# Performance work log

Hardware: AMD Instinct MI355X
Metric: run time of the kernel (lower is better)

Reference implementation:

```python
import jax, jax.numpy as jnp
import numpy as np

# dims
B, F, K = 64, 4096, 8
D_IN = D_SLOT = D_KVQ = 192
HID = 768
N_ITERS = 3
EPS = 1e-8
GROUPS = [(0, 1), (1, 7), (7, 8)]  # bg / fg / ag contiguous slot slices
SB_STRENGTH = 1.0
SB_SIGMA = 0.25
GRID = 64  # sqrt(F)


def _layernorm(x, g, b):
    m = jnp.mean(x, axis=-1, keepdims=True)
    v = jnp.mean(jnp.square(x - m), axis=-1, keepdims=True)
    return (x - m) * jax.lax.rsqrt(v + 1e-5) * g + b


def _gru_cell(x, h, Wih, Whh, bih, bhh):
    # torch.nn.GRUCell semantics; gate order r, z, n
    gi = x @ Wih.T + bih
    gh = h @ Whh.T + bhh
    ir, iz, i_n = jnp.split(gi, 3, axis=-1)
    hr, hz, h_n = jnp.split(gh, 3, axis=-1)
    r = jax.nn.sigmoid(ir + hr)
    z = jax.nn.sigmoid(iz + hz)
    n = jnp.tanh(i_n + r * h_n)
    return (1.0 - z) * n + z * h


def _token_coords():
    y = np.linspace(-1.0, 1.0, GRID, dtype=np.float32)
    x = np.linspace(-1.0, 1.0, GRID, dtype=np.float32)
    yy, xx = np.meshgrid(y, x, indexing='ij')
    return jnp.asarray(np.stack((xx, yy), axis=-1).reshape(F, 2))


def setup_inputs() -> dict:
    key = jax.random.key(0)
    ks = jax.random.split(key, 16)
    def n(i, shape, s=0.02):
        return jax.random.normal(ks[i], shape, jnp.float32) * s
    return dict(
        features=jax.random.normal(ks[0], (B, F, D_IN), jnp.float32),
        slots=jax.random.normal(ks[1], (B, K, D_SLOT), jnp.float32),
        Wk=n(2, (D_IN, D_KVQ)), Wv=n(3, (D_IN, D_KVQ)), Wq=n(4, (D_SLOT, D_KVQ)),
        ln_feat_g=jnp.ones(D_IN), ln_feat_b=jnp.zeros(D_IN),
        ln_slot_g=jnp.ones(D_SLOT), ln_slot_b=jnp.zeros(D_SLOT),
        gru_Wih=n(5, (3, 3 * D_SLOT, D_KVQ)), gru_Whh=n(6, (3, 3 * D_SLOT, D_SLOT)),
        gru_bih=n(7, (3, 3 * D_SLOT)), gru_bhh=n(8, (3, 3 * D_SLOT)),
        mlp_ln_g=jnp.ones((3, D_SLOT)), mlp_ln_b=jnp.zeros((3, D_SLOT)),
        mlp_W1=n(9, (3, D_SLOT, HID)), mlp_b1=n(10, (3, HID)),
        mlp_W2=n(11, (3, HID, D_SLOT)), mlp_b2=n(12, (3, D_SLOT)),
    )


def reference(features, slots, Wk, Wv, Wq, ln_feat_g, ln_feat_b, ln_slot_g,
              ln_slot_b, gru_Wih, gru_Whh, gru_bih, gru_bhh, mlp_ln_g,
              mlp_ln_b, mlp_W1, mlp_b1, mlp_W2, mlp_b2):
    coords = _token_coords()  # (F, 2)
    f = _layernorm(features, ln_feat_g, ln_feat_b)
    k = f @ Wk  # (B, F, Dk)
    v = f @ Wv
    scale = D_KVQ ** -0.5
    sigma2 = max(SB_SIGMA ** 2, 1e-8)
    prev_attn = None
    for _ in range(N_ITERS):
        slots_prev = slots
        q = _layernorm(slots, ln_slot_g, ln_slot_b) @ Wq  # (B, K, Dk)
        dots = jnp.einsum('bkd,bfd->bkf', q, k) * scale
        if prev_attn is not None and SB_STRENGTH > 0.0:
            w = prev_attn / (prev_attn.sum(-1, keepdims=True) + 1e-8)
            centers = jnp.einsum('bkf,fd->bkd', w, coords)  # (B, K, 2)
            diff = coords[None, None] - centers[:, :, None]  # (B, K, F, 2)
            dist2 = jnp.sum(diff * diff, axis=-1)
            dots = dots + SB_STRENGTH * (-dist2 / (2.0 * sigma2))
        attn = jax.nn.softmax(dots, axis=1)  # competition over slots
        prev_attn = attn
        w = attn / (attn.sum(-1, keepdims=True) + EPS)  # weighted mean over F
        updates = jnp.einsum('bkf,bfd->bkd', w, v)  # (B, K, Dk)
        outs = []
        for g, (s, e) in enumerate(GROUPS):
            u = updates[:, s:e].reshape(-1, D_KVQ)
            h_prev = slots_prev[:, s:e].reshape(-1, D_SLOT)
            h = _gru_cell(u, h_prev, gru_Wih[g], gru_Whh[g], gru_bih[g], gru_bhh[g])
            x = _layernorm(h, mlp_ln_g[g], mlp_ln_b[g])
            x = jax.nn.relu(x @ mlp_W1[g] + mlp_b1[g]) @ mlp_W2[g] + mlp_b2[g]
            outs.append((h + x).reshape(B, e - s, D_SLOT))
        slots = jnp.concatenate(outs, axis=1)
    return slots
```

## Files before the change

### kernel.cpp

```cpp
#include <hip/hip_runtime.h>

typedef unsigned short u16;
typedef unsigned int u32;

#define BB 64
#define FF 4096
#define DD 192
#define HH 768

typedef __attribute__((ext_vector_type(8))) __bf16 bf16x8;
typedef __attribute__((ext_vector_type(4))) float f32x4;

__device__ __forceinline__ float bf2f(u32 u) {
  union { u32 i; float f; } x; x.i = u << 16; return x.f;
}
__device__ __forceinline__ u16 f2bf(float f) {
  __bf16 h = (__bf16)f;
  return __builtin_bit_cast(u16, h);
}
__device__ __forceinline__ u32 pk2bf(float a, float b) {
  return (u32)f2bf(a) | ((u32)f2bf(b) << 16);
}
__device__ __forceinline__ float sigm(float x) { return 1.f / (1.f + __expf(-x)); }

__global__ void prep_wmod(const float* __restrict__ Wk, const float* __restrict__ Wv,
                          const float* __restrict__ g, const float* __restrict__ bb,
                          u16* __restrict__ wmodT, float* __restrict__ s1,
                          float* __restrict__ s0) {
  int n = blockIdx.x * 64 + threadIdx.x;
  const float* W = (n < DD) ? Wk : Wv;
  int col = (n < DD) ? n : n - DD;
  float a1 = 0.f, a0 = 0.f;
  for (int e = 0; e < DD; ++e) {
    float w = W[e * DD + col];
    u16 h = f2bf(g[e] * w);
    wmodT[n * DD + e] = h;
    a1 += bf2f(h);
    a0 += bb[e] * w;
  }
  s1[n] = a1; s0[n] = a0;
}

__global__ void prep_packw(const float* __restrict__ Wih, const float* __restrict__ Whh,
                           const float* __restrict__ W1, const float* __restrict__ W2,
                           u16* __restrict__ pWih, u16* __restrict__ pWhh,
                           u16* __restrict__ pW1, u16* __restrict__ pW2) {
  int which = blockIdx.y;
  int total, N, E;
  const float* src; u16* dst; int srcEmajor;
  if (which < 2) { total = 3 * 576 * 192; N = 576; E = 192; srcEmajor = 0;
                   src = which ? Whh : Wih; dst = which ? pWhh : pWih; }
  else if (which == 2) { total = 3 * 192 * 768; N = 768; E = 192; srcEmajor = 1;
                         src = W1; dst = pW1; }
  else { total = 3 * 768 * 192; N = 192; E = 768; srcEmajor = 1; src = W2; dst = pW2; }
  for (int idx = blockIdx.x * 256 + threadIdx.x; idx < total; idx += gridDim.x * 256) {
    int g = idx / (N * E), rem = idx % (N * E);
    int n, e;
    if (srcEmajor) { e = rem / N; n = rem % N; }
    else { n = rem / E; e = rem % E; }
    dst[((g * (E / 2) + (e >> 1)) * N + n) * 2 + (e & 1)] = f2bf(src[idx]);
  }
}

__global__ __launch_bounds__(256, 4) void proj_kernel(
    const float* __restrict__ feat, const u16* __restrict__ wmodT,
    const float* __restrict__ s1v, const float* __restrict__ s0v,
    u16* __restrict__ kc_, u16* __restrict__ vc_) {
  __shared__ __align__(16) u16 Ctile[4][2176];
  int tid = threadIdx.x;
  int w = tid >> 6, lane = tid & 63;
  int l15 = lane & 15, l4 = lane >> 4;
  long wtile = (long)blockIdx.x * 4 + w;
  long tok0 = wtile * 16;
  int bidx = (int)(wtile >> 8);
  int f0 = ((int)wtile & 255) * 16;
  char* ct = (char*)&Ctile[w][0];

  const float* fp = feat + (tok0 + l15) * DD + l4 * 8;
  float4 xa[6], xb[6];
  #pragma unroll
  for (int kk = 0; kk < 6; ++kk) {
    xa[kk] = *(const float4*)(fp + kk * 32);
    xb[kk] = *(const float4*)(fp + kk * 32 + 4);
  }
  float s = 0.f, s2 = 0.f;
  bf16x8 afr[6];
  #pragma unroll
  for (int kk = 0; kk < 6; ++kk) {
    float4 a = xa[kk], b = xb[kk];
    s += a.x + a.y + a.z + a.w + b.x + b.y + b.z + b.w;
    s2 += a.x * a.x + a.y * a.y + a.z * a.z + a.w * a.w +
          b.x * b.x + b.y * b.y + b.z * b.z + b.w * b.w;
    union { u32 u[4]; bf16x8 v; } cv;
    cv.u[0] = pk2bf(a.x, a.y); cv.u[1] = pk2bf(a.z, a.w);
    cv.u[2] = pk2bf(b.x, b.y); cv.u[3] = pk2bf(b.z, b.w);
    afr[kk] = cv.v;
  }
  s += __shfl_xor(s, 16); s2 += __shfl_xor(s2, 16);
  s += __shfl_xor(s, 32); s2 += __shfl_xor(s2, 32);
  float mu = s * (1.f / 192.f);
  float rstd = rsqrtf(s2 * (1.f / 192.f) - mu * mu + 1e-5f);
  float muv[4], rsv[4];
  #pragma unroll
  for (int j = 0; j < 4; ++j) {
    muv[j] = __shfl(mu, l4 * 4 + j);
    rsv[j] = __shfl(rstd, l4 * 4 + j);
  }

  #pragma unroll 1
  for (int grp = 0; grp < 4; ++grp) {
    f32x4 acc[6];
    #pragma unroll
    for (int nt = 0; nt < 6; ++nt) acc[nt] = (f32x4){0.f, 0.f, 0.f, 0.f};
    #pragma unroll
    for (int kk = 0; kk < 6; ++kk) {
      #pragma unroll
      for (int nt = 0; nt < 6; ++nt) {
        int col = grp * 96 + nt * 16 + l15;
        bf16x8 bfr = *(const bf16x8*)(wmodT + col * DD + kk * 32 + l4 * 8);
        acc[nt] = __builtin_amdgcn_mfma_f32_16x16x32_bf16(afr[kk], bfr, acc[nt], 0, 0, 0);
      }
    }
    if (grp < 2) {
      #pragma unroll
      for (int nt = 0; nt < 6; ++nt) {
        int col = nt * 16 + l15;
        float s1c = s1v[grp * 96 + col], s0c = s0v[grp * 96 + col];
        #pragma unroll
        for (int j = 0; j < 4; ++j) {
          int tau = l4 * 4 + j;
          u16 hv = f2bf(rsv[j] * (acc[nt][j] - muv[j] * s1c) + s0c);
          *(u16*)(ct + tau * 272 + (col >> 3) * 16 + (col & 7) * 2) = hv;
        }
      }
      #pragma unroll
      for (int it = 0; it < 3; ++it) {
        int fi = lane + it * 64;
        int g = fi >> 4, tau = fi & 15;
        uint4 val = *(uint4*)(ct + tau * 272 + g * 16);
        *(uint4*)(kc_ + (((long)wtile * 24 + grp * 12 + g) * 16 + tau) * 8) = val;
      }
    } else {
      #pragma unroll
      for (int nt = 0; nt < 6; ++nt) {
        int col = (grp - 2) * 96 + nt * 16 + l15;
        float s1c = s1v[col + 192], s0c = s0v[col + 192];
        int ntg = col >> 4;
        uint2 pk;
        pk.x = pk2bf(rsv[0] * (acc[nt][0] - muv[0] * s1c) + s0c,
                     rsv[1] * (acc[nt][1] - muv[1] * s1c) + s0c);
        pk.y = pk2bf(rsv[2] * (acc[nt][2] - muv[2] * s1c) + s0c,
                     rsv[3] * (acc[nt][3] - muv[3] * s1c) + s0c);
        u32 ox = __shfl_xor((int)pk.x, 16);
        u32 oy = __shfl_xor((int)pk.y, 16);
        if ((l4 & 1) == 0) {
          int t0 = f0 + l4 * 4;
          int g32 = t0 >> 5;
          int l4f = (t0 >> 3) & 3;
          uint4 val = {pk.x, pk.y, ox, oy};
          *(uint4*)(vc_ + ((((long)bidx * 128 + g32) * 12 + ntg) * 64 + l4f * 16 +
                           (col & 15)) * 8) = val;
        }
      }
    }
  }
}

__global__ __launch_bounds__(64) void qproj_kernel(
    const float* __restrict__ slots, const float* __restrict__ Wq,
    const float* __restrict__ g, const float* __restrict__ bb,
    float* __restrict__ qbuf, float* __restrict__ upd,
    float* __restrict__ asum_cur, float* __restrict__ cacc_cur) {
  __shared__ float ln[192];
  int bk = blockIdx.x;
  int lane = threadIdx.x;
  {
    int gtid = bk * 64 + lane;
    float4 z = {0.f, 0.f, 0.f, 0.f};
    if (gtid < 24576) ((float4*)upd)[gtid] = z;
    else if (gtid < 24576 + 128) ((float4*)asum_cur)[gtid - 24576] = z;
    else if (gtid < 24576 + 384) ((float4*)cacc_cur)[gtid - 24704] = z;
  }
  const float* x = slots + bk * DD;
  float v0 = x[lane], v1 = x[lane + 64], v2 = x[lane + 128];
  float s = v0 + v1 + v2, s2 = v0 * v0 + v1 * v1 + v2 * v2;
  #pragma unroll
  for (int m = 1; m < 64; m <<= 1) { s += __shfl_xor(s, m); s2 += __shfl_xor(s2, m); }
  float mu = s * (1.f / 192.f);
  float rstd = rsqrtf(s2 * (1.f / 192.f) - mu * mu + 1e-5f);
  ln[lane]       = (v0 - mu) * rstd * g[lane]       + bb[lane];
  ln[lane + 64]  = (v1 - mu) * rstd * g[lane + 64]  + bb[lane + 64];
  ln[lane + 128] = (v2 - mu) * rstd * g[lane + 128] + bb[lane + 128];
  __syncthreads();
  float a0 = 0.f, a1 = 0.f, a2 = 0.f;
  for (int e = 0; e < DD; ++e) {
    float le = ln[e];
    a0 += le * Wq[e * DD + lane];
    a1 += le * Wq[e * DD + lane + 64];
    a2 += le * Wq[e * DD + lane + 128];
  }
  const float scale = 0.07216878364870323f;
  qbuf[bk * DD + lane]       = a0 * scale;
  qbuf[bk * DD + lane + 64]  = a1 * scale;
  qbuf[bk * DD + lane + 128] = a2 * scale;
}

__global__ __launch_bounds__(256) void attnupd_kernel(
    const u16* __restrict__ kc_, const u16* __restrict__ vc_,
    const float* __restrict__ qbuf,
    const float* __restrict__ asum_prev, const float* __restrict__ cacc_prev,
    float* __restrict__ upd, float* __restrict__ asum_cur,
    float* __restrict__ cacc_cur, int have_bias) {
  __shared__ __align__(16) u16 qlds[16 * 192];
  __shared__ __align__(16) u16 attn_lds[16 * 256];
  int b = blockIdx.x;
  int chunk = blockIdx.y * 256;
  int tid = threadIdx.x;
  if (tid < 192) {
    int s = tid / 24, u = tid % 24;
    const float* qp = qbuf + (b * 8 + s) * DD + u * 8;
    uint4 p;
    p.x = pk2bf(qp[0], qp[1]);
    p.y = pk2bf(qp[2], qp[3]);
    p.z = pk2bf(qp[4], qp[5]);
    p.w = pk2bf(qp[6], qp[7]);
    *(uint4*)((char*)qlds + s * 384 + ((u ^ (s & 7)) << 4)) = p;
  } else {
    int t2 = tid - 192;
    #pragma unroll
    for (int i = 0; i < 3; ++i) {
      int idx = t2 * 3 + i;
      int s = 8 + idx / 24, u = idx % 24;
      *(uint4*)((char*)qlds + s * 384 + ((u ^ (s & 7)) << 4)) = (uint4){0, 0, 0, 0};
    }
    #pragma unroll
    for (int i = 0; i < 4; ++i)
      *(uint4*)((char*)attn_lds + 4096 + (t2 * 4 + i) * 16) = (uint4){0, 0, 0, 0};
  }
  __syncthreads();
  int w = tid >> 6, lane = tid & 63;
  int l15 = lane & 15, l4 = lane >> 4;
  bf16x8 qfr[6];
  #pragma unroll
  for (int kk = 0; kk < 6; ++kk) {
    int u = kk * 4 + l4;
    qfr[kk] = *(bf16x8*)((char*)qlds + l15 * 384 + ((u ^ (l15 & 7)) << 4));
  }
  float ax[4], ay[4], c0[4];
  #pragma unroll
  for (int j = 0; j < 4; ++j) {
    int s = l4 * 4 + j;
    if (have_bias && s < 8) {
      float inv = 1.f / (asum_prev[b * 8 + s] + 1e-8f);
      float cx = cacc_prev[(b * 8 + s) * 2] * inv;
      float cy = cacc_prev[(b * 8 + s) * 2 + 1] * inv;
      ax[j] = 16.f * cx; ay[j] = 16.f * cy; c0[j] = -8.f * (cx * cx + cy * cy);
    } else { ax[j] = 0.f; ay[j] = 0.f; c0[j] = 0.f; }
  }
  float pa[4], px[4], py[4];
  #pragma unroll
  for (int j = 0; j < 4; ++j) { pa[j] = 0.f; px[j] = 0.f; py[j] = 0.f; }
  for (int tile = w; tile < 16; tile += 4) {
    int t0 = chunk + tile * 16;
    long Tg = (long)b * 256 + (t0 >> 4);
    const u16* kp = kc_ + (Tg * 24 + l4) * 128 + l15 * 8;
    f32x4 acc = (f32x4){0.f, 0.f, 0.f, 0.f};
    #pragma unroll
    for (int kk = 0; kk < 6; ++kk) {
      bf16x8 bfr = *(const bf16x8*)(kp + kk * 512);
      acc = __builtin_amdgcn_mfma_f32_16x16x32_bf16(qfr[kk], bfr, acc, 0, 0, 0);
    }
    int t = t0 + l15;
    float x = -1.f + (float)(t & 63) * (2.f / 63.f);
    float y = -1.f + (float)(t >> 6) * (2.f / 63.f);
    float m8r2 = -8.f * (x * x + y * y);
    float d4[4];
    #pragma unroll
    for (int j = 0; j < 4; ++j)
      d4[j] = acc[j] + (have_bias ? (ax[j] * x + ay[j] * y + c0[j] + m8r2) : 0.f);
    float o4[4];
    #pragma unroll
    for (int j = 0; j < 4; ++j) o4[j] = __shfl_xor(d4[j], 16);
    float mx = fmaxf(fmaxf(fmaxf(d4[0], d4[1]), fmaxf(d4[2], d4[3])),
                     fmaxf(fmaxf(o4[0], o4[1]), fmaxf(o4[2], o4[3])));
    float e4[4];
    float sum = 0.f;
    #pragma unroll
    for (int j = 0; j < 4; ++j) { e4[j] = __expf(d4[j] - mx); sum += e4[j]; }
    #pragma unroll
    for (int j = 0; j < 4; ++j) sum += __expf(o4[j] - mx);
    float inv = 1.f / sum;
    if (l4 < 2) {
      int tl = tile * 16 + l15;
      #pragma unroll
      for (int j = 0; j < 4; ++j) {
        float a = e4[j] * inv;
        int s = l4 * 4 + j;
        *(u16*)((char*)attn_lds + ((s * 512 + tl * 2) ^ ((s & 7) << 4))) = f2bf(a);
        pa[j] += a; px[j] += a * x; py[j] += a * y;
      }
    }
  }
  #pragma unroll
  for (int m = 1; m < 16; m <<= 1) {
    #pragma unroll
    for (int j = 0; j < 4; ++j) {
      pa[j] += __shfl_xor(pa[j], m);
      px[j] += __shfl_xor(px[j], m);
      py[j] += __shfl_xor(py[j], m);
    }
  }
  if (l15 == 0 && l4 < 2) {
    #pragma unroll
    for (int j = 0; j < 4; ++j) {
      int s = l4 * 4 + j;
      atomicAdd(&asum_cur[b * 8 + s], pa[j]);
      atomicAdd(&cacc_cur[(b * 8 + s) * 2], px[j]);
      atomicAdd(&cacc_cur[(b * 8 + s) * 2 + 1], py[j]);
    }
  }
  __syncthreads();
  int g32base = chunk >> 5;
  #pragma unroll
  for (int ni = 0; ni < 3; ++ni) {
    int nt = w * 3 + ni;
    f32x4 acc = (f32x4){0.f, 0.f, 0.f, 0.f};
    const u16* vp = vc_ + ((((long)b * 128 + g32base) * 12 + nt) * 64 + l4 * 16 + l15) * 8;
    #pragma unroll
    for (int gl = 0; gl < 8; ++gl) {
      int tl0 = gl * 32 + l4 * 8;
      bf16x8 afr = *(bf16x8*)((char*)attn_lds + ((l15 * 512 + tl0 * 2) ^ ((l15 & 7) << 4)));
      bf16x8 bfr = *(const bf16x8*)(vp + gl * 12 * 64 * 8);
      acc = __builtin_amdgcn_mfma_f32_16x16x32_bf16(afr, bfr, acc, 0, 0, 0);
    }
    if (l4 < 2) {
      #pragma unroll
      for (int j = 0; j < 4; ++j) {
        int s = l4 * 4 + j;
        atomicAdd(&upd[((long)b * 8 + s) * DD + nt * 16 + l15], acc[j]);
      }
    }
  }
}

template <int M>
__device__ void gru_body(int b0, int g, int srow,
                         float* u_l, float* h_l, float* gi_l, float* gh_l,
                         float* hn_l, float* ln_l, float* x1_l, float* out_l, float* st,
                         const float* __restrict__ upd, const float* __restrict__ asum,
                         const float* __restrict__ sin_,
                         const u16* __restrict__ pWih, const u16* __restrict__ pWhh,
                         const float* __restrict__ bih, const float* __restrict__ bhh,
                         const float* __restrict__ mlng, const float* __restrict__ mlnb,
                         const u16* __restrict__ pW1, const float* __restrict__ b1,
                         const u16* __restrict__ pW2, const float* __restrict__ b2,
                         float* __restrict__ sout) {
  int tid = threadIdx.x;
  for (int idx = tid; idx < M * 192; idx += 768) {
    int row = idx / 192, d = idx % 192;
    int gr = b0 * 8 + srow + row;
    float inv = 1.f / (asum[gr] + 1e-8f);
    u_l[row * 192 + d] = upd[gr * DD + d] * inv;
    h_l[row * 192 + d] = sin_[gr * DD + d];
  }
  __syncthreads();
  if (tid < 576) {
    int c = tid;
    const u16* wih = pWih + (size_t)g * 96 * 1152 + c * 2;
    const u16* whh = pWhh + (size_t)g * 96 * 1152 + c * 2;
    float ai[M], ah[M];
    #pragma unroll
    for (int r = 0; r < M; ++r) { ai[r] = 0.f; ah[r] = 0.f; }
    #pragma unroll 4
    for (int e2 = 0; e2 < 96; ++e2) {
      u32 wi = *(const u32*)(wih + e2 * 1152);
      u32 wh = *(const u32*)(whh + e2 * 1152);
      float wi0 = bf2f(wi & 0xffffu), wi1 = bf2f(wi >> 16);
      float wh0 = bf2f(wh & 0xffffu), wh1 = bf2f(wh >> 16);
      #pragma unroll
      for (int r = 0; r < M; ++r) {
        ai[r] += wi0 * u_l[r * 192 + e2 * 2] + wi1 * u_l[r * 192 + e2 * 2 + 1];
        ah[r] += wh0 * h_l[r * 192 + e2 * 2] + wh1 * h_l[r * 192 + e2 * 2 + 1];
      }
    }
    #pragma unroll
    for (int r = 0; r < M; ++r) { gi_l[r * 576 + c] = ai[r]; gh_l[r * 576 + c] = ah[r]; }
  }
  __syncthreads();
  if (tid < M * 192) {
    int row = tid / 192, uu = tid % 192;
    const float* bihg = bih + g * 576;
    const float* bhhg = bhh + g * 576;
    float r_ = sigm(gi_l[row * 576 + uu] + bihg[uu] + gh_l[row * 576 + uu] + bhhg[uu]);
    float z_ = sigm(gi_l[row * 576 + 192 + uu] + bihg[192 + uu] +
                    gh_l[row * 576 + 192 + uu] + bhhg[192 + uu]);
    float nn = gi_l[row * 576 + 384 + uu] + bihg[384 + uu] +
               r_ * (gh_l[row * 576 + 384 + uu] + bhhg[384 + uu]);
    float t = 1.f - 2.f / (__expf(2.f * nn) + 1.f);
    hn_l[row * 192 + uu] = (1.f - z_) * t + z_ * h_l[row * 192 + uu];
  }
  __syncthreads();
  {
    int wv = tid >> 6, lane = tid & 63;
    if (wv < M) {
      float v0 = hn_l[wv * 192 + lane], v1 = hn_l[wv * 192 + lane + 64],
            v2 = hn_l[wv * 192 + lane + 128];
      float s = v0 + v1 + v2, sq = v0 * v0 + v1 * v1 + v2 * v2;
      #pragma unroll
      for (int m = 1; m < 64; m <<= 1) { s += __shfl_xor(s, m); sq += __shfl_xor(sq, m); }
      if (lane == 0) {
        float mu = s * (1.f / 192.f);
        st[wv * 2] = mu;
        st[wv * 2 + 1] = rsqrtf(sq * (1.f / 192.f) - mu * mu + 1e-5f);
      }
    }
  }
  __syncthreads();
  if (tid < M * 192) {
    int row = tid / 192, uu = tid % 192;
    ln_l[row * 192 + uu] = (hn_l[row * 192 + uu] - st[row * 2]) * st[row * 2 + 1] *
                               mlng[g * DD + uu] + mlnb[g * DD + uu];
  }
  __syncthreads();
  {
    int c = tid;
    const u16* w1 = pW1 + (size_t)g * 96 * 1536 + c * 2;
    float a[M];
    #pragma unroll
    for (int r = 0; r < M; ++r) a[r] = 0.f;
    #pragma unroll 4
    for (int e2 = 0; e2 < 96; ++e2) {
      u32 wp = *(const u32*)(w1 + e2 * 1536);
      float w0 = bf2f(wp & 0xffffu), w1f = bf2f(wp >> 16);
      #pragma unroll
      for (int r = 0; r < M; ++r)
        a[r] += w0 * ln_l[r * 192 + e2 * 2] + w1f * ln_l[r * 192 + e2 * 2 + 1];
    }
    float bc = b1[g * HH + c];
    #pragma unroll
    for (int r = 0; r < M; ++r) x1_l[r * 768 + c] = fmaxf(a[r] + bc, 0.f);
  }
  if (tid < M * 192) {
    int row = tid / 192, uu = tid % 192;
    out_l[row * 192 + uu] = hn_l[row * 192 + uu] + b2[g * DD + uu];
  }
  __syncthreads();
  {
    int c = tid % 192, ks = tid / 192;
    const u16* w2 = pW2 + (size_t)g * 384 * 384 + c * 2;
    float a[M];
    #pragma unroll
    for (int r = 0; r < M; ++r) a[r] = 0.f;
    #pragma unroll 4
    for (int e2 = ks * 96; e2 < ks * 96 + 96; ++e2) {
      u32 wp = *(const u32*)(w2 + e2 * 384);
      float w0 = bf2f(wp & 0xffffu), w1f = bf2f(wp >> 16);
      #pragma unroll
      for (int r = 0; r < M; ++r)
        a[r] += w0 * x1_l[r * 768 + e2 * 2] + w1f * x1_l[r * 768 + e2 * 2 + 1];
    }
    #pragma unroll
    for (int r = 0; r < M; ++r) atomicAdd(&out_l[r * 192 + c], a[r]);
  }
  __syncthreads();
  if (tid < M * 192) {
    int row = tid / 192, d = tid % 192;
    sout[(b0 * 8 + srow + row) * DD + d] = out_l[row * 192 + d];
  }
}

__global__ __launch_bounds__(768) void gru_kernel(
    const float* __restrict__ upd, const float* __restrict__ asum,
    const float* __restrict__ sin_,
    const u16* __restrict__ pWih, const u16* __restrict__ pWhh,
    const float* __restrict__ bih, const float* __restrict__ bhh,
    const float* __restrict__ mlng, const float* __restrict__ mlnb,
    const u16* __restrict__ pW1, const float* __restrict__ b1,
    const u16* __restrict__ pW2, const float* __restrict__ b2,
    float* __restrict__ sout) {
  __shared__ float u_l[3 * 192], h_l[3 * 192], gi_l[3 * 576], gh_l[3 * 576];
  __shared__ float hn_l[3 * 192], ln_l[3 * 192], x1_l[3 * 768], out_l[3 * 192], st[8];
  int b = blockIdx.x, y = blockIdx.y;
  if (y == 0)
    gru_body<1>(b, 0, 0, u_l, h_l, gi_l, gh_l, hn_l, ln_l, x1_l, out_l, st,
                upd, asum, sin_, pWih, pWhh, bih, bhh, mlng, mlnb, pW1, b1, pW2, b2, sout);
  else if (y == 1)
    gru_body<1>(b, 2, 7, u_l, h_l, gi_l, gh_l, hn_l, ln_l, x1_l, out_l, st,
                upd, asum, sin_, pWih, pWhh, bih, bhh, mlng, mlnb, pW1, b1, pW2, b2, sout);
  else if (y == 2)
    gru_body<3>(b, 1, 1, u_l, h_l, gi_l, gh_l, hn_l, ln_l, x1_l, out_l, st,
                upd, asum, sin_, pWih, pWhh, bih, bhh, mlng, mlnb, pW1, b1, pW2, b2, sout);
  else
    gru_body<3>(b, 1, 4, u_l, h_l, gi_l, gh_l, hn_l, ln_l, x1_l, out_l, st,
                upd, asum, sin_, pWih, pWhh, bih, bhh, mlng, mlnb, pW1, b1, pW2, b2, sout);
}

extern "C" void kernel_launch(void* const* d_in, const int* in_sizes, int n_in,
                              void* d_out, int out_size, void* d_ws, size_t ws_size,
                              hipStream_t stream) {
  const float* feat = (const float*)d_in[0];
  const float* slots = (const float*)d_in[1];
  const float* Wk = (const float*)d_in[2];
  const float* Wv = (const float*)d_in[3];
  const float* Wq = (const float*)d_in[4];
  const float* lfg = (const float*)d_in[5];
  const float* lfb = (const float*)d_in[6];
  const float* lsg = (const float*)d_in[7];
  const float* lsb = (const float*)d_in[8];
  const float* gWih = (const float*)d_in[9];
  const float* gWhh = (const float*)d_in[10];
  const float* gbih = (const float*)d_in[11];
  const float* gbhh = (const float*)d_in[12];
  const float* mlng = (const float*)d_in[13];
  const float* mlnb = (const float*)d_in[14];
  const float* W1 = (const float*)d_in[15];
  const float* b1 = (const float*)d_in[16];
  const float* W2 = (const float*)d_in[17];
  const float* b2 = (const float*)d_in[18];
  float* out = (float*)d_out;

  char* ws = (char*)d_ws;
  size_t off = 0;
  auto alloc = [&](size_t bytes) {
    void* p = ws + off;
    off += (bytes + 255) & ~(size_t)255;
    return p;
  };
  u16* kc_    = (u16*)alloc((size_t)BB * FF * DD * 2);
  u16* vc_    = (u16*)alloc((size_t)BB * DD * FF * 2);
  float* qbuf = (float*)alloc((size_t)BB * 8 * DD * 4);
  float* upd  = (float*)alloc((size_t)BB * 8 * DD * 4);
  float* slA  = (float*)alloc((size_t)BB * 8 * DD * 4);
  float* slB  = (float*)alloc((size_t)BB * 8 * DD * 4);
  float* asum0 = (float*)alloc(BB * 8 * 4);
  float* asum1 = (float*)alloc(BB * 8 * 4);
  float* cacc0 = (float*)alloc(BB * 8 * 2 * 4);
  float* cacc1 = (float*)alloc(BB * 8 * 2 * 4);
  u16* wmodT  = (u16*)alloc(384 * DD * 2);
  float* s1   = (float*)alloc(384 * 4);
  float* s0   = (float*)alloc(384 * 4);
  u16* pWih   = (u16*)alloc((size_t)3 * 576 * DD * 2);
  u16* pWhh   = (u16*)alloc((size_t)3 * 576 * DD * 2);
  u16* pW1    = (u16*)alloc((size_t)3 * DD * HH * 2);
  u16* pW2    = (u16*)alloc((size_t)3 * HH * DD * 2);

  prep_wmod<<<6, 64, 0, stream>>>(Wk, Wv, lfg, lfb, wmodT, s1, s0);
  prep_packw<<<dim3(432, 4), 256, 0, stream>>>(gWih, gWhh, W1, W2, pWih, pWhh, pW1, pW2);
  proj_kernel<<<BB * FF / 64, 256, 0, stream>>>(feat, wmodT, s1, s0, kc_, vc_);

  const float* sin_ = slots;
  float* souts[3] = {slA, slB, out};
  float* asums[2] = {asum0, asum1};
  float* caccs[2] = {cacc0, cacc1};
  for (int it = 0; it < 3; ++it) {
    int cur = it & 1, prev = cur ^ 1;
    qproj_kernel<<<BB * 8, 64, 0, stream>>>(sin_, Wq, lsg, lsb, qbuf,
                                            upd, asums[cur], caccs[cur]);
    attnupd_kernel<<<dim3(BB, 16), 256, 0, stream>>>(kc_, vc_, qbuf, asums[prev],
                                                     caccs[prev], upd, asums[cur],
                                                     caccs[cur], it > 0 ? 1 : 0);
    gru_kernel<<<dim3(BB, 4), 768, 0, stream>>>(upd, asums[cur], sin_, pWih, pWhh,
                                                gbih, gbhh, mlng, mlnb, pW1, b1, pW2, b2,
                                                souts[it]);
    sin_ = souts[it];
  }
}
```

Measured before the change: 593.4 us.

## Fold K/V projections into queries and updates, attend over raw normalized features

Replaces the up-front MFMA projection of LayerNorm'd features into K and V. The features are now only converted to bf16 in two layouts, with per-token mean and rstd stored separately. Queries are pushed through Wk (times the LN gain) so attention runs directly on raw bf16 features with an affine LN correction. Weighted feature sums are projected through Wv inside the GRU kernel using a gamma/mu correction term. This drops the large projection GEMM and moves the per-slot projections into small kernels, at the cost of extra stats reads, an extra atomic, and a serial 192-wide dot product per output in qproj and gru.

```diff
diff --git a/kernel.cpp b/kernel.cpp
--- a/kernel.cpp
+++ b/kernel.cpp
@@ -23,22 +23,19 @@
 }
 __device__ __forceinline__ float sigm(float x) { return 1.f / (1.f + __expf(-x)); }
 
-__global__ void prep_wmod(const float* __restrict__ Wk, const float* __restrict__ Wv,
-                          const float* __restrict__ g, const float* __restrict__ bb,
-                          u16* __restrict__ wmodT, float* __restrict__ s1,
-                          float* __restrict__ s0) {
-  int n = blockIdx.x * 64 + threadIdx.x;
-  const float* W = (n < DD) ? Wk : Wv;
-  int col = (n < DD) ? n : n - DD;
-  float a1 = 0.f, a0 = 0.f;
+__global__ void prep_vw(const float* __restrict__ Wk, const float* __restrict__ Wv,
+                        const float* __restrict__ g, const float* __restrict__ bb,
+                        float* __restrict__ Wvm, float* __restrict__ s0v,
+                        float* __restrict__ s0k) {
+  int d = threadIdx.x;
+  float av = 0.f, ak = 0.f;
   for (int e = 0; e < DD; ++e) {
-    float w = W[e * DD + col];
-    u16 h = f2bf(g[e] * w);
-    wmodT[n * DD + e] = h;
-    a1 += bf2f(h);
-    a0 += bb[e] * w;
-  }
-  s1[n] = a1; s0[n] = a0;
+    float wv = Wv[e * DD + d];
+    Wvm[e * DD + d] = g[e] * wv;
+    av += bb[e] * wv;
+    ak += bb[e] * Wk[e * DD + d];
+  }
+  s0v[d] = av; s0k[d] = ak;
 }
 
 __global__ void prep_packw(const float* __restrict__ Wih, const float* __restrict__ Whh,
@@ -62,124 +59,74 @@
   }
 }
 
-__global__ __launch_bounds__(256, 4) void proj_kernel(
-    const float* __restrict__ feat, const u16* __restrict__ wmodT,
-    const float* __restrict__ s1v, const float* __restrict__ s0v,
-    u16* __restrict__ kc_, u16* __restrict__ vc_) {
-  __shared__ __align__(16) u16 Ctile[4][2176];
+__global__ __launch_bounds__(256) void fconv(const float* __restrict__ feat,
+                                             u16* __restrict__ fb, u16* __restrict__ fd,
+                                             float2* __restrict__ stats) {
+  __shared__ __align__(16) u16 flds[64 * 192];
   int tid = threadIdx.x;
-  int w = tid >> 6, lane = tid & 63;
-  int l15 = lane & 15, l4 = lane >> 4;
-  long wtile = (long)blockIdx.x * 4 + w;
-  long tok0 = wtile * 16;
-  int bidx = (int)(wtile >> 8);
-  int f0 = ((int)wtile & 255) * 16;
-  char* ct = (char*)&Ctile[w][0];
-
-  const float* fp = feat + (tok0 + l15) * DD + l4 * 8;
-  float4 xa[6], xb[6];
-  #pragma unroll
-  for (int kk = 0; kk < 6; ++kk) {
-    xa[kk] = *(const float4*)(fp + kk * 32);
-    xb[kk] = *(const float4*)(fp + kk * 32 + 4);
-  }
+  int blk = blockIdx.x;
+  int r = tid >> 2, p = tid & 3;
+  long t = (long)blk * 64 + r;
+  const float4* src = (const float4*)(feat + t * DD) + p * 12;
   float s = 0.f, s2 = 0.f;
-  bf16x8 afr[6];
-  #pragma unroll
-  for (int kk = 0; kk < 6; ++kk) {
-    float4 a = xa[kk], b = xb[kk];
+  long Tg = t >> 4; int tau = (int)(t & 15);
+  #pragma unroll
+  for (int i = 0; i < 6; ++i) {
+    float4 a = src[i * 2], b = src[i * 2 + 1];
     s += a.x + a.y + a.z + a.w + b.x + b.y + b.z + b.w;
     s2 += a.x * a.x + a.y * a.y + a.z * a.z + a.w * a.w +
           b.x * b.x + b.y * b.y + b.z * b.z + b.w * b.w;
-    union { u32 u[4]; bf16x8 v; } cv;
-    cv.u[0] = pk2bf(a.x, a.y); cv.u[1] = pk2bf(a.z, a.w);
-    cv.u[2] = pk2bf(b.x, b.y); cv.u[3] = pk2bf(b.z, b.w);
-    afr[kk] = cv.v;
-  }
-  s += __shfl_xor(s, 16); s2 += __shfl_xor(s2, 16);
-  s += __shfl_xor(s, 32); s2 += __shfl_xor(s2, 32);
-  float mu = s * (1.f / 192.f);
-  float rstd = rsqrtf(s2 * (1.f / 192.f) - mu * mu + 1e-5f);
-  float muv[4], rsv[4];
-  #pragma unroll
-  for (int j = 0; j < 4; ++j) {
-    muv[j] = __shfl(mu, l4 * 4 + j);
-    rsv[j] = __shfl(rstd, l4 * 4 + j);
-  }
-
-  #pragma unroll 1
-  for (int grp = 0; grp < 4; ++grp) {
-    f32x4 acc[6];
-    #pragma unroll
-    for (int nt = 0; nt < 6; ++nt) acc[nt] = (f32x4){0.f, 0.f, 0.f, 0.f};
-    #pragma unroll
-    for (int kk = 0; kk < 6; ++kk) {
-      #pragma unroll
-      for (int nt = 0; nt < 6; ++nt) {
-        int col = grp * 96 + nt * 16 + l15;
-        bf16x8 bfr = *(const bf16x8*)(wmodT + col * DD + kk * 32 + l4 * 8);
-        acc[nt] = __builtin_amdgcn_mfma_f32_16x16x32_bf16(afr[kk], bfr, acc[nt], 0, 0, 0);
-      }
-    }
-    if (grp < 2) {
-      #pragma unroll
-      for (int nt = 0; nt < 6; ++nt) {
-        int col = nt * 16 + l15;
-        float s1c = s1v[grp * 96 + col], s0c = s0v[grp * 96 + col];
-        #pragma unroll
-        for (int j = 0; j < 4; ++j) {
-          int tau = l4 * 4 + j;
-          u16 hv = f2bf(rsv[j] * (acc[nt][j] - muv[j] * s1c) + s0c);
-          *(u16*)(ct + tau * 272 + (col >> 3) * 16 + (col & 7) * 2) = hv;
-        }
-      }
-      #pragma unroll
-      for (int it = 0; it < 3; ++it) {
-        int fi = lane + it * 64;
-        int g = fi >> 4, tau = fi & 15;
-        uint4 val = *(uint4*)(ct + tau * 272 + g * 16);
-        *(uint4*)(kc_ + (((long)wtile * 24 + grp * 12 + g) * 16 + tau) * 8) = val;
-      }
-    } else {
-      #pragma unroll
-      for (int nt = 0; nt < 6; ++nt) {
-        int col = (grp - 2) * 96 + nt * 16 + l15;
-        float s1c = s1v[col + 192], s0c = s0v[col + 192];
-        int ntg = col >> 4;
-        uint2 pk;
-        pk.x = pk2bf(rsv[0] * (acc[nt][0] - muv[0] * s1c) + s0c,
-                     rsv[1] * (acc[nt][1] - muv[1] * s1c) + s0c);
-        pk.y = pk2bf(rsv[2] * (acc[nt][2] - muv[2] * s1c) + s0c,
-                     rsv[3] * (acc[nt][3] - muv[3] * s1c) + s0c);
-        u32 ox = __shfl_xor((int)pk.x, 16);
-        u32 oy = __shfl_xor((int)pk.y, 16);
-        if ((l4 & 1) == 0) {
-          int t0 = f0 + l4 * 4;
-          int g32 = t0 >> 5;
-          int l4f = (t0 >> 3) & 3;
-          uint4 val = {pk.x, pk.y, ox, oy};
-          *(uint4*)(vc_ + ((((long)bidx * 128 + g32) * 12 + ntg) * 64 + l4f * 16 +
-                           (col & 15)) * 8) = val;
-        }
-      }
-    }
+    uint4 v;
+    v.x = pk2bf(a.x, a.y); v.y = pk2bf(a.z, a.w);
+    v.z = pk2bf(b.x, b.y); v.w = pk2bf(b.z, b.w);
+    int u = p * 6 + i;
+    *(uint4*)(fb + ((Tg * 24 + u) * 16 + tau) * 8) = v;
+    *(uint4*)((char*)flds + r * 384 + p * 96 + i * 16) = v;
+  }
+  s += __shfl_xor(s, 1); s2 += __shfl_xor(s2, 1);
+  s += __shfl_xor(s, 2); s2 += __shfl_xor(s2, 2);
+  if (p == 0) {
+    float mu = s * (1.f / 192.f);
+    float rstd = rsqrtf(s2 * (1.f / 192.f) - mu * mu + 1e-5f);
+    stats[t] = make_float2(rstd, mu);
+  }
+  __syncthreads();
+  int b = blk >> 6;
+  #pragma unroll
+  for (int i = 0; i < 6; ++i) {
+    int idx = tid + i * 256;
+    int tg8 = idx / 192, d = idx % 192;
+    u16 h[8];
+    #pragma unroll
+    for (int j = 0; j < 8; ++j) h[j] = flds[(tg8 * 8 + j) * 192 + d];
+    uint4 v;
+    v.x = (u32)h[0] | ((u32)h[1] << 16);
+    v.y = (u32)h[2] | ((u32)h[3] << 16);
+    v.z = (u32)h[4] | ((u32)h[5] << 16);
+    v.w = (u32)h[6] | ((u32)h[7] << 16);
+    int g32 = (blk & 63) * 2 + (tg8 >> 2);
+    int l4f = tg8 & 3;
+    *(uint4*)(fd + ((((long)b * 128 + g32) * 12 + (d >> 4)) * 64 + l4f * 16 +
+                    (d & 15)) * 8) = v;
   }
 }
 
 __global__ __launch_bounds__(64) void qproj_kernel(
     const float* __restrict__ slots, const float* __restrict__ Wq,
-    const float* __restrict__ g, const float* __restrict__ bb,
-    float* __restrict__ qbuf, float* __restrict__ upd,
-    float* __restrict__ asum_cur, float* __restrict__ cacc_cur) {
+    const float* __restrict__ lsg, const float* __restrict__ lsb,
+    const float* __restrict__ Wk, const float* __restrict__ lfg,
+    const float* __restrict__ s0k,
+    u16* __restrict__ pbuf, float* __restrict__ pab,
+    float* __restrict__ U, float* __restrict__ scal_cur) {
   __shared__ float ln[192];
   int bk = blockIdx.x;
+  int b = bk >> 3, sl = bk & 7;
   int lane = threadIdx.x;
   {
     int gtid = bk * 64 + lane;
     float4 z = {0.f, 0.f, 0.f, 0.f};
-    if (gtid < 24576) ((float4*)upd)[gtid] = z;
-    else if (gtid < 24576 + 128) ((float4*)asum_cur)[gtid - 24576] = z;
-    else if (gtid < 24576 + 384) ((float4*)cacc_cur)[gtid - 24704] = z;
+    if (gtid < 24576) ((float4*)U)[gtid] = z;
+    else if (gtid < 24576 + 512) ((float4*)scal_cur)[gtid - 24576] = z;
   }
   const float* x = slots + bk * DD;
   float v0 = x[lane], v1 = x[lane + 64], v2 = x[lane + 128];
@@ -188,9 +135,9 @@
   for (int m = 1; m < 64; m <<= 1) { s += __shfl_xor(s, m); s2 += __shfl_xor(s2, m); }
   float mu = s * (1.f / 192.f);
   float rstd = rsqrtf(s2 * (1.f / 192.f) - mu * mu + 1e-5f);
-  ln[lane]       = (v0 - mu) * rstd * g[lane]       + bb[lane];
-  ln[lane + 64]  = (v1 - mu) * rstd * g[lane + 64]  + bb[lane + 64];
-  ln[lane + 128] = (v2 - mu) * rstd * g[lane + 128] + bb[lane + 128];
+  ln[lane]       = (v0 - mu) * rstd * lsg[lane]       + lsb[lane];
+  ln[lane + 64]  = (v1 - mu) * rstd * lsg[lane + 64]  + lsb[lane + 64];
+  ln[lane + 128] = (v2 - mu) * rstd * lsg[lane + 128] + lsb[lane + 128];
   __syncthreads();
   float a0 = 0.f, a1 = 0.f, a2 = 0.f;
   for (int e = 0; e < DD; ++e) {
@@ -199,44 +146,54 @@
     a1 += le * Wq[e * DD + lane + 64];
     a2 += le * Wq[e * DD + lane + 128];
   }
+  __syncthreads();
   const float scale = 0.07216878364870323f;
-  qbuf[bk * DD + lane]       = a0 * scale;
-  qbuf[bk * DD + lane + 64]  = a1 * scale;
-  qbuf[bk * DD + lane + 128] = a2 * scale;
-}
-
-__global__ __launch_bounds__(256) void attnupd_kernel(
-    const u16* __restrict__ kc_, const u16* __restrict__ vc_,
-    const float* __restrict__ qbuf,
-    const float* __restrict__ asum_prev, const float* __restrict__ cacc_prev,
-    float* __restrict__ upd, float* __restrict__ asum_cur,
-    float* __restrict__ cacc_cur, int have_bias) {
-  __shared__ __align__(16) u16 qlds[16 * 192];
+  ln[lane] = a0 * scale; ln[lane + 64] = a1 * scale; ln[lane + 128] = a2 * scale;
+  __syncthreads();
+  float al = 0.f, be = 0.f;
+  u16 pb[3];
+  #pragma unroll
+  for (int k3 = 0; k3 < 3; ++k3) {
+    int d = lane + k3 * 64;
+    const float* wr = Wk + (size_t)d * DD;
+    float pd = 0.f;
+    for (int e = 0; e < DD; ++e) pd += wr[e] * ln[e];
+    pd *= lfg[d];
+    u16 h = f2bf(pd);
+    pb[k3] = h;
+    al += bf2f(h);
+    be += s0k[d] * ln[d];
+  }
+  #pragma unroll
+  for (int m = 1; m < 64; m <<= 1) { al += __shfl_xor(al, m); be += __shfl_xor(be, m); }
+  #pragma unroll
+  for (int k3 = 0; k3 < 3; ++k3)
+    pbuf[(b * 16 + sl) * DD + lane + k3 * 64] = pb[k3];
+  if (lane < 24) *(uint4*)(pbuf + (b * 16 + 8 + sl) * DD + lane * 8) = (uint4){0, 0, 0, 0};
+  if (lane == 0) { pab[bk * 2] = al; pab[bk * 2 + 1] = be; }
+}
+
+__global__ __launch_bounds__(256) void attnpv_kernel(
+    const u16* __restrict__ fb, const u16* __restrict__ fd,
+    const u16* __restrict__ pbuf, const float* __restrict__ pab,
+    const float2* __restrict__ stats,
+    const float* __restrict__ scal_prev,
+    float* __restrict__ U, float* __restrict__ scal_cur, int have_bias) {
+  __shared__ __align__(16) u16 plds[16 * 192];
   __shared__ __align__(16) u16 attn_lds[16 * 256];
   int b = blockIdx.x;
   int chunk = blockIdx.y * 256;
   int tid = threadIdx.x;
-  if (tid < 192) {
-    int s = tid / 24, u = tid % 24;
-    const float* qp = qbuf + (b * 8 + s) * DD + u * 8;
-    uint4 p;
-    p.x = pk2bf(qp[0], qp[1]);
-    p.y = pk2bf(qp[2], qp[3]);
-    p.z = pk2bf(qp[4], qp[5]);
-    p.w = pk2bf(qp[6], qp[7]);
-    *(uint4*)((char*)qlds + s * 384 + ((u ^ (s & 7)) << 4)) = p;
-  } else {
-    int t2 = tid - 192;
-    #pragma unroll
-    for (int i = 0; i < 3; ++i) {
-      int idx = t2 * 3 + i;
-      int s = 8 + idx / 24, u = idx % 24;
-      *(uint4*)((char*)qlds + s * 384 + ((u ^ (s & 7)) << 4)) = (uint4){0, 0, 0, 0};
-    }
-    #pragma unroll
-    for (int i = 0; i < 4; ++i)
-      *(uint4*)((char*)attn_lds + 4096 + (t2 * 4 + i) * 16) = (uint4){0, 0, 0, 0};
-  }
+  #pragma unroll
+  for (int i = 0; i < 2; ++i) {
+    int g = tid + i * 256;
+    if (g < 384) {
+      int s = g / 24, u = g % 24;
+      uint4 v = *(const uint4*)(pbuf + ((b * 16 + s) * DD + u * 8));
+      *(uint4*)((char*)plds + s * 384 + ((u ^ (s & 7)) << 4)) = v;
+    }
+  }
+  *(uint4*)((char*)attn_lds + 4096 + tid * 16) = (uint4){0, 0, 0, 0};
   __syncthreads();
   int w = tid >> 6, lane = tid & 63;
   int l15 = lane & 15, l4 = lane >> 4;
@@ -244,26 +201,30 @@
   #pragma unroll
   for (int kk = 0; kk < 6; ++kk) {
     int u = kk * 4 + l4;
-    qfr[kk] = *(bf16x8*)((char*)qlds + l15 * 384 + ((u ^ (l15 & 7)) << 4));
-  }
-  float ax[4], ay[4], c0[4];
+    qfr[kk] = *(bf16x8*)((char*)plds + l15 * 384 + ((u ^ (l15 & 7)) << 4));
+  }
+  float ax[4], ay[4], c0[4], av[4], bv[4];
   #pragma unroll
   for (int j = 0; j < 4; ++j) {
     int s = l4 * 4 + j;
-    if (have_bias && s < 8) {
-      float inv = 1.f / (asum_prev[b * 8 + s] + 1e-8f);
-      float cx = cacc_prev[(b * 8 + s) * 2] * inv;
-      float cy = cacc_prev[(b * 8 + s) * 2 + 1] * inv;
-      ax[j] = 16.f * cx; ay[j] = 16.f * cy; c0[j] = -8.f * (cx * cx + cy * cy);
-    } else { ax[j] = 0.f; ay[j] = 0.f; c0[j] = 0.f; }
-  }
-  float pa[4], px[4], py[4];
-  #pragma unroll
-  for (int j = 0; j < 4; ++j) { pa[j] = 0.f; px[j] = 0.f; py[j] = 0.f; }
+    if (s < 8) {
+      av[j] = pab[(b * 8 + s) * 2];
+      bv[j] = pab[(b * 8 + s) * 2 + 1];
+      if (have_bias) {
+        float inv = 1.f / (scal_prev[(b * 8 + s) * 4] + 1e-8f);
+        float cx = scal_prev[(b * 8 + s) * 4 + 1] * inv;
+        float cy = scal_prev[(b * 8 + s) * 4 + 2] * inv;
+        ax[j] = 16.f * cx; ay[j] = 16.f * cy; c0[j] = -8.f * (cx * cx + cy * cy);
+      } else { ax[j] = 0.f; ay[j] = 0.f; c0[j] = 0.f; }
+    } else { av[j] = 0.f; bv[j] = 0.f; ax[j] = 0.f; ay[j] = 0.f; c0[j] = 0.f; }
+  }
+  float pa[4], px[4], py[4], pg[4];
+  #pragma unroll
+  for (int j = 0; j < 4; ++j) { pa[j] = 0.f; px[j] = 0.f; py[j] = 0.f; pg[j] = 0.f; }
   for (int tile = w; tile < 16; tile += 4) {
     int t0 = chunk + tile * 16;
     long Tg = (long)b * 256 + (t0 >> 4);
-    const u16* kp = kc_ + (Tg * 24 + l4) * 128 + l15 * 8;
+    const u16* kp = fb + (Tg * 24 + l4) * 128 + l15 * 8;
     f32x4 acc = (f32x4){0.f, 0.f, 0.f, 0.f};
     #pragma unroll
     for (int kk = 0; kk < 6; ++kk) {
@@ -271,13 +232,16 @@
       acc = __builtin_amdgcn_mfma_f32_16x16x32_bf16(qfr[kk], bfr, acc, 0, 0, 0);
     }
     int t = t0 + l15;
+    float2 st = stats[((long)b << 12) + t];
+    float rstd = st.x, muv = st.y;
     float x = -1.f + (float)(t & 63) * (2.f / 63.f);
     float y = -1.f + (float)(t >> 6) * (2.f / 63.f);
     float m8r2 = -8.f * (x * x + y * y);
     float d4[4];
     #pragma unroll
     for (int j = 0; j < 4; ++j)
-      d4[j] = acc[j] + (have_bias ? (ax[j] * x + ay[j] * y + c0[j] + m8r2) : 0.f);
+      d4[j] = rstd * acc[j] - rstd * muv * av[j] + bv[j] +
+              (have_bias ? (ax[j] * x + ay[j] * y + c0[j] + m8r2) : 0.f);
     float o4[4];
     #pragma unroll
     for (int j = 0; j < 4; ++j) o4[j] = __shfl_xor(d4[j], 16);
@@ -295,9 +259,11 @@
       #pragma unroll
       for (int j = 0; j < 4; ++j) {
         float a = e4[j] * inv;
+        u16 wr = f2bf(a * rstd);
         int s = l4 * 4 + j;
-        *(u16*)((char*)attn_lds + ((s * 512 + tl * 2) ^ ((s & 7) << 4))) = f2bf(a);
+        *(u16*)((char*)attn_lds + ((s * 512 + tl * 2) ^ ((s & 7) << 4))) = wr;
         pa[j] += a; px[j] += a * x; py[j] += a * y;
+        pg[j] += bf2f(wr) * muv;
       }
     }
   }
@@ -308,15 +274,17 @@
       pa[j] += __shfl_xor(pa[j], m);
       px[j] += __shfl_xor(px[j], m);
       py[j] += __shfl_xor(py[j], m);
+      pg[j] += __shfl_xor(pg[j], m);
     }
   }
   if (l15 == 0 && l4 < 2) {
     #pragma unroll
     for (int j = 0; j < 4; ++j) {
       int s = l4 * 4 + j;
-      atomicAdd(&asum_cur[b * 8 + s], pa[j]);
-      atomicAdd(&cacc_cur[(b * 8 + s) * 2], px[j]);
-      atomicAdd(&cacc_cur[(b * 8 + s) * 2 + 1], py[j]);
+      atomicAdd(&scal_cur[(b * 8 + s) * 4], pa[j]);
+      atomicAdd(&scal_cur[(b * 8 + s) * 4 + 1], px[j]);
+      atomicAdd(&scal_cur[(b * 8 + s) * 4 + 2], py[j]);
+      atomicAdd(&scal_cur[(b * 8 + s) * 4 + 3], pg[j]);
     }
   }
   __syncthreads();
@@ -325,7 +293,7 @@
   for (int ni = 0; ni < 3; ++ni) {
     int nt = w * 3 + ni;
     f32x4 acc = (f32x4){0.f, 0.f, 0.f, 0.f};
-    const u16* vp = vc_ + ((((long)b * 128 + g32base) * 12 + nt) * 64 + l4 * 16 + l15) * 8;
+    const u16* vp = fd + ((((long)b * 128 + g32base) * 12 + nt) * 64 + l4 * 16 + l15) * 8;
     #pragma unroll
     for (int gl = 0; gl < 8; ++gl) {
       int tl0 = gl * 32 + l4 * 8;
@@ -337,7 +305,7 @@
       #pragma unroll
       for (int j = 0; j < 4; ++j) {
         int s = l4 * 4 + j;
-        atomicAdd(&upd[((long)b * 8 + s) * DD + nt * 16 + l15], acc[j]);
+        atomicAdd(&U[((long)b * 8 + s) * DD + nt * 16 + l15], acc[j]);
       }
     }
   }
@@ -347,7 +315,8 @@
 __device__ void gru_body(int b0, int g, int srow,
                          float* u_l, float* h_l, float* gi_l, float* gh_l,
                          float* hn_l, float* ln_l, float* x1_l, float* out_l, float* st,
-                         const float* __restrict__ upd, const float* __restrict__ asum,
+                         const float* __restrict__ U, const float* __restrict__ scal,
+                         const float* __restrict__ Wvm, const float* __restrict__ s0v,
                          const float* __restrict__ sin_,
                          const u16* __restrict__ pWih, const u16* __restrict__ pWhh,
                          const float* __restrict__ bih, const float* __restrict__ bhh,
@@ -359,9 +328,20 @@
   for (int idx = tid; idx < M * 192; idx += 768) {
     int row = idx / 192, d = idx % 192;
     int gr = b0 * 8 + srow + row;
-    float inv = 1.f / (asum[gr] + 1e-8f);
-    u_l[row * 192 + d] = upd[gr * DD + d] * inv;
+    hn_l[row * 192 + d] = U[(long)gr * DD + d];
     h_l[row * 192 + d] = sin_[gr * DD + d];
+  }
+  __syncthreads();
+  if (tid < M * 192) {
+    int row = tid / 192, d = tid % 192;
+    int gr = b0 * 8 + srow + row;
+    float asum = scal[gr * 4], gam = scal[gr * 4 + 3];
+    float inv = 1.f / (asum + 1e-8f);
+    float acc = asum * s0v[d];
+    const float* ur = hn_l + row * 192;
+    #pragma unroll 4
+    for (int e = 0; e < DD; ++e) acc += (ur[e] - gam) * Wvm[e * DD + d];
+    u_l[row * 192 + d] = acc * inv;
   }
   __syncthreads();
   if (tid < 576) {
@@ -470,7 +450,8 @@
 }
 
 __global__ __launch_bounds__(768) void gru_kernel(
-    const float* __restrict__ upd, const float* __restrict__ asum,
+    const float* __restrict__ U, const float* __restrict__ scal,
+    const float* __restrict__ Wvm, const float* __restrict__ s0v,
     const float* __restrict__ sin_,
     const u16* __restrict__ pWih, const u16* __restrict__ pWhh,
     const float* __restrict__ bih, const float* __restrict__ bhh,
@@ -483,16 +464,20 @@
   int b = blockIdx.x, y = blockIdx.y;
   if (y == 0)
     gru_body<1>(b, 0, 0, u_l, h_l, gi_l, gh_l, hn_l, ln_l, x1_l, out_l, st,
-                upd, asum, sin_, pWih, pWhh, bih, bhh, mlng, mlnb, pW1, b1, pW2, b2, sout);
+                U, scal, Wvm, s0v, sin_, pWih, pWhh, bih, bhh, mlng, mlnb,
+                pW1, b1, pW2, b2, sout);
   else if (y == 1)
     gru_body<1>(b, 2, 7, u_l, h_l, gi_l, gh_l, hn_l, ln_l, x1_l, out_l, st,
-                upd, asum, sin_, pWih, pWhh, bih, bhh, mlng, mlnb, pW1, b1, pW2, b2, sout);
+                U, scal, Wvm, s0v, sin_, pWih, pWhh, bih, bhh, mlng, mlnb,
+                pW1, b1, pW2, b2, sout);
   else if (y == 2)
     gru_body<3>(b, 1, 1, u_l, h_l, gi_l, gh_l, hn_l, ln_l, x1_l, out_l, st,
-                upd, asum, sin_, pWih, pWhh, bih, bhh, mlng, mlnb, pW1, b1, pW2, b2, sout);
+                U, scal, Wvm, s0v, sin_, pWih, pWhh, bih, bhh, mlng, mlnb,
+                pW1, b1, pW2, b2, sout);
   else
     gru_body<3>(b, 1, 4, u_l, h_l, gi_l, gh_l, hn_l, ln_l, x1_l, out_l, st,
-                upd, asum, sin_, pWih, pWhh, bih, bhh, mlng, mlnb, pW1, b1, pW2, b2, sout);
+                U, scal, Wvm, s0v, sin_, pWih, pWhh, bih, bhh, mlng, mlnb,
+                pW1, b1, pW2, b2, sout);
 }
 
 extern "C" void kernel_launch(void* const* d_in, const int* in_sizes, int n_in,
@@ -526,42 +511,41 @@
     off += (bytes + 255) & ~(size_t)255;
     return p;
   };
-  u16* kc_    = (u16*)alloc((size_t)BB * FF * DD * 2);
-  u16* vc_    = (u16*)alloc((size_t)BB * DD * FF * 2);
-  float* qbuf = (float*)alloc((size_t)BB * 8 * DD * 4);
-  float* upd  = (float*)alloc((size_t)BB * 8 * DD * 4);
-  float* slA  = (float*)alloc((size_t)BB * 8 * DD * 4);
-  float* slB  = (float*)alloc((size_t)BB * 8 * DD * 4);
-  float* asum0 = (float*)alloc(BB * 8 * 4);
-  float* asum1 = (float*)alloc(BB * 8 * 4);
-  float* cacc0 = (float*)alloc(BB * 8 * 2 * 4);
-  float* cacc1 = (float*)alloc(BB * 8 * 2 * 4);
-  u16* wmodT  = (u16*)alloc(384 * DD * 2);
-  float* s1   = (float*)alloc(384 * 4);
-  float* s0   = (float*)alloc(384 * 4);
-  u16* pWih   = (u16*)alloc((size_t)3 * 576 * DD * 2);
-  u16* pWhh   = (u16*)alloc((size_t)3 * 576 * DD * 2);
-  u16* pW1    = (u16*)alloc((size_t)3 * DD * HH * 2);
-  u16* pW2    = (u16*)alloc((size_t)3 * HH * DD * 2);
-
-  prep_wmod<<<6, 64, 0, stream>>>(Wk, Wv, lfg, lfb, wmodT, s1, s0);
+  u16* fb      = (u16*)alloc((size_t)BB * FF * DD * 2);
+  u16* fd      = (u16*)alloc((size_t)BB * DD * FF * 2);
+  float2* stats = (float2*)alloc((size_t)BB * FF * 8);
+  u16* pbuf    = (u16*)alloc((size_t)BB * 16 * DD * 2);
+  float* pab   = (float*)alloc((size_t)BB * 8 * 2 * 4);
+  float* U     = (float*)alloc((size_t)BB * 8 * DD * 4);
+  float* slA   = (float*)alloc((size_t)BB * 8 * DD * 4);
+  float* slB   = (float*)alloc((size_t)BB * 8 * DD * 4);
+  float* scal0 = (float*)alloc(BB * 8 * 4 * 4);
+  float* scal1 = (float*)alloc(BB * 8 * 4 * 4);
+  float* Wvm   = (float*)alloc((size_t)DD * DD * 4);
+  float* s0v   = (float*)alloc(DD * 4);
+  float* s0k   = (float*)alloc(DD * 4);
+  u16* pWih    = (u16*)alloc((size_t)3 * 576 * DD * 2);
+  u16* pWhh    = (u16*)alloc((size_t)3 * 576 * DD * 2);
+  u16* pW1     = (u16*)alloc((size_t)3 * DD * HH * 2);
+  u16* pW2     = (u16*)alloc((size_t)3 * HH * DD * 2);
+
+  prep_vw<<<1, 192, 0, stream>>>(Wk, Wv, lfg, lfb, Wvm, s0v, s0k);
   prep_packw<<<dim3(432, 4), 256, 0, stream>>>(gWih, gWhh, W1, W2, pWih, pWhh, pW1, pW2);
-  proj_kernel<<<BB * FF / 64, 256, 0, stream>>>(feat, wmodT, s1, s0, kc_, vc_);
+  fconv<<<BB * FF / 64, 256, 0, stream>>>(feat, fb, fd, stats);
 
   const float* sin_ = slots;
   float* souts[3] = {slA, slB, out};
-  float* asums[2] = {asum0, asum1};
-  float* caccs[2] = {cacc0, cacc1};
+  float* scals[2] = {scal0, scal1};
   for (int it = 0; it < 3; ++it) {
     int cur = it & 1, prev = cur ^ 1;
-    qproj_kernel<<<BB * 8, 64, 0, stream>>>(sin_, Wq, lsg, lsb, qbuf,
-                                            upd, asums[cur], caccs[cur]);
-    attnupd_kernel<<<dim3(BB, 16), 256, 0, stream>>>(kc_, vc_, qbuf, asums[prev],
-                                                     caccs[prev], upd, asums[cur],
-                                                     caccs[cur], it > 0 ? 1 : 0);
-    gru_kernel<<<dim3(BB, 4), 768, 0, stream>>>(upd, asums[cur], sin_, pWih, pWhh,
-                                                gbih, gbhh, mlng, mlnb, pW1, b1, pW2, b2,
-                                                souts[it]);
+    qproj_kernel<<<BB * 8, 64, 0, stream>>>(sin_, Wq, lsg, lsb, Wk, lfg, s0k,
+                                            pbuf, pab, U, scals[cur]);
+    attnpv_kernel<<<dim3(BB, 16), 256, 0, stream>>>(fb, fd, pbuf, pab, stats,
+                                                    scals[prev], U, scals[cur],
+                                                    it > 0 ? 1 : 0);
+    gru_kernel<<<dim3(BB, 4), 768, 0, stream>>>(U, scals[cur], Wvm, s0v, sin_,
+                                                pWih, pWhh, gbih, gbhh, mlng, mlnb,
+                                                pW1, b1, pW2, b2, souts[it]);
     sin_ = souts[it];
   }
 }
```

After: 519.2 us. 1.14x faster.
